# Kernel optimization log

Measured on AMD Instinct MI355X. Metric: run time of the kernel, lower is better.

Reference implementation:

```python
import jax, jax.numpy as jnp
import numpy as np

N = 100000   # nodes
E = 1600000  # edges (avg degree 16)
D = 128      # in_dim == hidden
L = 3        # num_layers
G = 512      # graphs in batch


def setup_inputs() -> dict:
    key = jax.random.key(0)
    ks = jax.random.split(key, 14)
    s = 0.05
    return {
        "x": jax.random.normal(ks[0], (N, D), jnp.float32),
        "edge_index": jax.random.randint(ks[1], (2, E), 0, N, dtype=jnp.int32),
        "batch": jnp.sort(jax.random.randint(ks[2], (N,), 0, G, dtype=jnp.int32)),
        "W1": jax.random.normal(ks[3], (L, D, D), jnp.float32) * s,
        "b1": jax.random.normal(ks[4], (L, D), jnp.float32) * s,
        "W2": jax.random.normal(ks[5], (L, D, D), jnp.float32) * s,
        "b2": jax.random.normal(ks[6], (L, D), jnp.float32) * s,
        "gamma": jax.random.uniform(ks[7], (L, D), jnp.float32, 0.5, 1.5),
        "beta": jax.random.normal(ks[8], (L, D), jnp.float32) * s,
        "run_mean": jax.random.normal(ks[9], (L, D), jnp.float32) * s,
        "run_var": jax.random.uniform(ks[10], (L, D), jnp.float32, 0.5, 1.5),
        "eps": jnp.zeros((L,), jnp.float32),
        "lin1_W": jax.random.normal(ks[11], (D, D), jnp.float32) * s,
        "lin1_b": jax.random.normal(ks[12], (D,), jnp.float32) * s,
    }


def _bn(h, g, b, m, v):
    # BatchNorm1d in eval mode (running stats)
    return (h - m) * jax.lax.rsqrt(v + 1e-5) * g + b


def reference(x, edge_index, batch, W1, b1, W2, b2, gamma, beta,
              run_mean, run_var, eps, lin1_W, lin1_b):
    n = x.shape[0]
    src, dst = edge_index[0], edge_index[1]
    h = x
    for l in range(L):  # small fixed layer count
        # GINConv: sum-aggregate neighbor features then (1+eps)*self + agg
        agg = jax.ops.segment_sum(h[src], dst, num_segments=n)  # [N, D]
        z = (1.0 + eps[l]) * h + agg
        z = jax.nn.relu(z @ W1[l] + b1[l])
        z = jax.nn.relu(z @ W2[l] + b2[l])
        h = _bn(z, gamma[l], beta[l], run_mean[l], run_var[l])
    # global_mean_pool over graph ids
    counts = jax.ops.segment_sum(jnp.ones((n,), h.dtype), batch, num_segments=G)
    pooled = jax.ops.segment_sum(h, batch, num_segments=G)
    pooled = pooled / jnp.maximum(counts, 1.0)[:, None]  # [G, D]
    # lin1 + ReLU (dropout is identity in eval)
    return jax.nn.relu(pooled @ lin1_W + lin1_b)
```

## Files before the change

kernel.cpp:

```cpp
#include <hip/hip_runtime.h>
#include <hip/hip_bf16.h>

#define NN 100000
#define NE 1600000
#define DD 128
#define NL 3
#define NG 512
#define NBLK ((NN + 255) / 256)
#define CSRP (NE + 8 * NN)

#define CONV_BLKS 12501
#define PREPW_BLKS 384
#define DEG_BLKS  391
#define INIT_BLKS (CONV_BLKS + PREPW_BLKS + DEG_BLKS)

typedef __attribute__((ext_vector_type(8))) short bf16x8;
typedef __attribute__((ext_vector_type(4))) float f32x4;

__device__ __forceinline__ unsigned short f2bf(float f) {
    union { float f; unsigned int u; } x; x.f = f;
    unsigned int r = x.u + 0x7FFFu + ((x.u >> 16) & 1u);
    return (unsigned short)(r >> 16);
}
__device__ __forceinline__ float bf2f(unsigned short u) {
    union { unsigned int u; float f; } x; x.u = ((unsigned int)u) << 16;
    return x.f;
}
__device__ __forceinline__ float bflo(unsigned int v) { return bf2f((unsigned short)(v & 0xffffu)); }
__device__ __forceinline__ float bfhi(unsigned int v) { return bf2f((unsigned short)(v >> 16)); }
__device__ __forceinline__ unsigned cvtpk(float lo, float hi) {
    unsigned r;
    asm("v_cvt_pk_bf16_f32 %0, %1, %2" : "=v"(r) : "v"(lo), "v"(hi));
    return r;
}

__global__ __launch_bounds__(256) void init_all(const float* __restrict__ x,
                                                unsigned short* __restrict__ h0,
                                                unsigned short* __restrict__ h1,
                                                const float* __restrict__ W1,
                                                const float* __restrict__ W2,
                                                unsigned short* __restrict__ wbf,
                                                int* __restrict__ deg) {
    int bb = blockIdx.x;
    if (bb < CONV_BLKS) {
        long long t = (long long)bb * 256 + threadIdx.x;
        long long base = t * 4;
        if (base < (long long)NN * DD) {
            float4 v = *reinterpret_cast<const float4*>(x + base);
            ushort4 p;
            p.x = f2bf(v.x); p.y = f2bf(v.y); p.z = f2bf(v.z); p.w = f2bf(v.w);
            *reinterpret_cast<ushort4*>(h0 + base) = p;
        } else if (base < (long long)(NN + 1) * DD) {
            ushort4 z = {0, 0, 0, 0};
            *reinterpret_cast<ushort4*>(h0 + base) = z;
            *reinterpret_cast<ushort4*>(h1 + base) = z;
        }
        return;
    }
    bb -= CONV_BLKS;
    if (bb < PREPW_BLKS) {
        int idx = bb * 256 + threadIdx.x;
        int k = idx & 127;
        int n = (idx >> 7) & 127;
        int w = (idx >> 14) & 1;
        int l = idx >> 15;
        const float* src = w ? W2 : W1;
        wbf[idx] = f2bf(src[(l * DD + k) * DD + n]);
        return;
    }
    bb -= PREPW_BLKS;
    int i = bb * 256 + threadIdx.x;
    if (i < NN) deg[i] = 0;
}

__global__ __launch_bounds__(256) void hist_deg(const int* __restrict__ ei,
                                                int* __restrict__ deg) {
    unsigned int e = blockIdx.x * 256u + threadIdx.x;
    atomicAdd(&deg[ei[NE + e]], 1);
}

__global__ __launch_bounds__(256) void scan1(const int* __restrict__ deg,
                                             int* __restrict__ rp,
                                             int* __restrict__ part) {
    __shared__ int s[256];
    int tid = threadIdx.x;
    int i = blockIdx.x * 256 + tid;
    int v = 0;
    if (i < NN) v = (deg[i] + 7) & ~7;
    s[tid] = v;
    __syncthreads();
    for (int o = 1; o < 256; o <<= 1) {
        int t = (tid >= o) ? s[tid - o] : 0;
        __syncthreads();
        s[tid] += t;
        __syncthreads();
    }
    if (i < NN) rp[i] = s[tid] - v;
    if (tid == 255) part[blockIdx.x] = s[255];
}

__global__ __launch_bounds__(256) void scan23(int* __restrict__ rp,
                                              const int* __restrict__ part,
                                              const int* __restrict__ deg,
                                              int* __restrict__ cnt,
                                              int* __restrict__ csr) {
    __shared__ int red[256];
    int tid = threadIdx.x;
    int bid = blockIdx.x;
    int s = 0;
    for (int i = tid; i < bid; i += 256) s += part[i];
    red[tid] = s;
    __syncthreads();
    for (int o = 128; o > 0; o >>= 1) {
        if (tid < o) red[tid] += red[tid + o];
        __syncthreads();
    }
    int base = red[0];
    int i = bid * 256 + tid;
    if (i < NN) {
        int val = rp[i] + base;
        rp[i] = val;
        cnt[i] = 0;
        int d = deg[i];
        int pd = (d + 7) & ~7;
        for (int j = val + d; j < val + pd; ++j) csr[j] = NN;
        if (i == NN - 1) rp[NN] = val + pd;
    }
}

__global__ __launch_bounds__(256) void fill_csr(const int* __restrict__ ei,
                                                const int* __restrict__ rp,
                                                int* __restrict__ cnt,
                                                int* __restrict__ csr) {
    unsigned int e = blockIdx.x * 256u + threadIdx.x;
    int s = ei[e];
    int d = ei[NE + e];
    int pos = atomicAdd(&cnt[d], 1);
    csr[rp[d] + pos] = s;
}

__global__ __launch_bounds__(256) void layer_fused(
    const unsigned short* __restrict__ hin,
    const int* __restrict__ rp,
    const int* __restrict__ csr,
    const unsigned short* __restrict__ w1t,
    const unsigned short* __restrict__ w2t,
    const float* __restrict__ b1,
    const float* __restrict__ b2,
    const float* __restrict__ gamma,
    const float* __restrict__ beta,
    const float* __restrict__ rmean,
    const float* __restrict__ rvar,
    const float* __restrict__ epsv,
    unsigned short* __restrict__ hout)
{
    __shared__ unsigned short z_lds[16 * 136];
    const int tid = threadIdx.x;
    const int lane = tid & 63;
    const int wave = tid >> 6;
    const int gid = lane >> 4;
    const int lg = lane & 15;
    const int row0 = blockIdx.x * 16;
    const float epl = 1.0f + epsv[0];
    const size_t lgo = (size_t)lg * 8;

#define ACC8(v) do { \
    acc[0] += bflo((v).x); acc[1] += bfhi((v).x); \
    acc[2] += bflo((v).y); acc[3] += bfhi((v).y); \
    acc[4] += bflo((v).z); acc[5] += bfhi((v).z); \
    acc[6] += bflo((v).w); acc[7] += bfhi((v).w); } while (0)

    const int rbase = row0 + (wave << 2);
    int pv = (lane < 5) ? rp[rbase + lane] : 0;
    const int st = __shfl(pv, gid);
    const int en = __shfl(pv, gid + 1);
    const int myrow = rbase + gid;

    float acc[8];
    {
        uint4 sv = *reinterpret_cast<const uint4*>(hin + (size_t)myrow * DD + lgo);
        acc[0] = epl * bflo(sv.x); acc[1] = epl * bfhi(sv.x);
        acc[2] = epl * bflo(sv.y); acc[3] = epl * bfhi(sv.y);
        acc[4] = epl * bflo(sv.z); acc[5] = epl * bfhi(sv.z);
        acc[6] = epl * bflo(sv.w); acc[7] = epl * bfhi(sv.w);
    }
    for (int c0 = st; c0 < en; c0 += 8) {
        int4 idA = *reinterpret_cast<const int4*>(csr + c0);
        int4 idB = *reinterpret_cast<const int4*>(csr + c0 + 4);
        uint4 v0 = *reinterpret_cast<const uint4*>(hin + (size_t)idA.x * DD + lgo);
        uint4 v1 = *reinterpret_cast<const uint4*>(hin + (size_t)idA.y * DD + lgo);
        uint4 v2 = *reinterpret_cast<const uint4*>(hin + (size_t)idA.z * DD + lgo);
        uint4 v3 = *reinterpret_cast<const uint4*>(hin + (size_t)idA.w * DD + lgo);
        uint4 v4 = *reinterpret_cast<const uint4*>(hin + (size_t)idB.x * DD + lgo);
        uint4 v5 = *reinterpret_cast<const uint4*>(hin + (size_t)idB.y * DD + lgo);
        uint4 v6 = *reinterpret_cast<const uint4*>(hin + (size_t)idB.z * DD + lgo);
        uint4 v7 = *reinterpret_cast<const uint4*>(hin + (size_t)idB.w * DD + lgo);
        ACC8(v0); ACC8(v1); ACC8(v2); ACC8(v3);
        ACC8(v4); ACC8(v5); ACC8(v6); ACC8(v7);
    }
    {
        uint4 pk;
        pk.x = cvtpk(acc[0], acc[1]);
        pk.y = cvtpk(acc[2], acc[3]);
        pk.z = cvtpk(acc[4], acc[5]);
        pk.w = cvtpk(acc[6], acc[7]);
        *reinterpret_cast<uint4*>(&z_lds[((wave << 2) + gid) * 136 + lg * 8]) = pk;
    }
    __syncthreads();

    const int l15 = lane & 15;
    const int kq = lane >> 4;
    const int colbase = wave << 5;

    bf16x8 afr[4];
    #pragma unroll
    for (int kk = 0; kk < 4; ++kk)
        afr[kk] = *reinterpret_cast<const bf16x8*>(&z_lds[l15 * 136 + kk * 32 + kq * 8]);

    f32x4 acc4[2];
    #pragma unroll
    for (int nt = 0; nt < 2; ++nt) acc4[nt] = (f32x4){0.f, 0.f, 0.f, 0.f};
    #pragma unroll
    for (int nt = 0; nt < 2; ++nt) {
        #pragma unroll
        for (int kk = 0; kk < 4; ++kk) {
            bf16x8 bfr = *reinterpret_cast<const bf16x8*>(
                w1t + (colbase + nt * 16 + l15) * DD + kk * 32 + kq * 8);
            acc4[nt] = __builtin_amdgcn_mfma_f32_16x16x32_bf16(afr[kk], bfr, acc4[nt], 0, 0, 0);
        }
    }
    __syncthreads();

    #pragma unroll
    for (int nt = 0; nt < 2; ++nt) {
        int col = colbase + nt * 16 + l15;
        float bv = b1[col];
        #pragma unroll
        for (int r = 0; r < 4; ++r) {
            int zr = kq * 4 + r;
            float v = acc4[nt][r] + bv;
            v = v > 0.f ? v : 0.f;
            z_lds[zr * 136 + col] = f2bf(v);
        }
    }
    __syncthreads();

    #pragma unroll
    for (int kk = 0; kk < 4; ++kk)
        afr[kk] = *reinterpret_cast<const bf16x8*>(&z_lds[l15 * 136 + kk * 32 + kq * 8]);
    #pragma unroll
    for (int nt = 0; nt < 2; ++nt) acc4[nt] = (f32x4){0.f, 0.f, 0.f, 0.f};
    #pragma unroll
    for (int nt = 0; nt < 2; ++nt) {
        #pragma unroll
        for (int kk = 0; kk < 4; ++kk) {
            bf16x8 bfr = *reinterpret_cast<const bf16x8*>(
                w2t + (colbase + nt * 16 + l15) * DD + kk * 32 + kq * 8);
            acc4[nt] = __builtin_amdgcn_mfma_f32_16x16x32_bf16(afr[kk], bfr, acc4[nt], 0, 0, 0);
        }
    }

    #pragma unroll
    for (int nt = 0; nt < 2; ++nt) {
        int col = colbase + nt * 16 + l15;
        float bv = b2[col];
        float ga = gamma[col];
        float be = beta[col];
        float mu = rmean[col];
        float inv = rsqrtf(rvar[col] + 1e-5f);
        #pragma unroll
        for (int r = 0; r < 4; ++r) {
            int zr = kq * 4 + r;
            float v = acc4[nt][r] + bv;
            v = v > 0.f ? v : 0.f;
            v = (v - mu) * inv * ga + be;
            hout[(size_t)(row0 + zr) * DD + col] = f2bf(v);
        }
    }
#undef ACC8
}

__global__ __launch_bounds__(256) void pool_final(const unsigned short* __restrict__ h,
                                                  const int* __restrict__ batch,
                                                  const float* __restrict__ W,
                                                  const float* __restrict__ b,
                                                  float* __restrict__ out) {
    int g = blockIdx.x;
    int t = threadIdx.x;
    int c2 = t & 63;
    int qu = t >> 6;

    int lo = 0, hi = NN;
    while (lo < hi) { int mid = (lo + hi) >> 1; if (batch[mid] < g) lo = mid + 1; else hi = mid; }
    int start = lo;
    hi = NN;
    while (lo < hi) { int mid = (lo + hi) >> 1; if (batch[mid] < g + 1) lo = mid + 1; else hi = mid; }
    int end = lo;

    float ax = 0.f, ay = 0.f;
    for (int i = start + qu; i < end; i += 4) {
        unsigned u = *reinterpret_cast<const unsigned*>(h + (size_t)i * DD + c2 * 2);
        ax += bflo(u); ay += bfhi(u);
    }

    __shared__ float ps[4][DD];
    ps[qu][c2 * 2] = ax;
    ps[qu][c2 * 2 + 1] = ay;
    __syncthreads();
    if (t < DD) {
        float inv = 1.0f / fmaxf((float)(end - start), 1.0f);
        ps[0][t] = (ps[0][t] + ps[1][t] + ps[2][t] + ps[3][t]) * inv;
    }
    __syncthreads();
    if (t < DD) {
        float o = b[t];
        #pragma unroll 8
        for (int k = 0; k < DD; ++k)
            o += ps[0][k] * W[k * DD + t];
        out[(size_t)g * DD + t] = fmaxf(o, 0.f);
    }
}

extern "C" void kernel_launch(void* const* d_in, const int* in_sizes, int n_in,
                              void* d_out, int out_size, void* d_ws, size_t ws_size,
                              hipStream_t stream) {
    const float* x     = (const float*)d_in[0];
    const int*   ei    = (const int*)d_in[1];
    const int*   batch = (const int*)d_in[2];
    const float* W1    = (const float*)d_in[3];
    const float* b1    = (const float*)d_in[4];
    const float* W2    = (const float*)d_in[5];
    const float* b2    = (const float*)d_in[6];
    const float* gamma = (const float*)d_in[7];
    const float* beta  = (const float*)d_in[8];
    const float* rmean = (const float*)d_in[9];
    const float* rvar  = (const float*)d_in[10];
    const float* eps   = (const float*)d_in[11];
    const float* lin1W = (const float*)d_in[12];
    const float* lin1b = (const float*)d_in[13];
    float* out = (float*)d_out;

    char* ws = (char*)d_ws;
    size_t off = 0;
    auto alloc = [&](size_t bytes) {
        void* p = ws + off;
        off = (off + bytes + 255) & ~(size_t)255;
        return p;
    };
    unsigned short* h0  = (unsigned short*)alloc((size_t)(NN + 1) * DD * 2);
    unsigned short* h1  = (unsigned short*)alloc((size_t)(NN + 1) * DD * 2);
    int* rp   = (int*)alloc((size_t)(NN + 1) * 4);
    int* deg  = (int*)alloc((size_t)NN * 4);
    int* cnt  = (int*)alloc((size_t)NN * 4);
    int* part = (int*)alloc(512 * 4);
    int* csr  = (int*)alloc((size_t)CSRP * 4);
    unsigned short* wbf = (unsigned short*)alloc((size_t)NL * 2 * DD * DD * 2);

    init_all<<<INIT_BLKS, 256, 0, stream>>>(x, h0, h1, W1, W2, wbf, deg);

    hist_deg<<<NE / 256, 256, 0, stream>>>(ei, deg);
    scan1<<<NBLK, 256, 0, stream>>>(deg, rp, part);
    scan23<<<NBLK, 256, 0, stream>>>(rp, part, deg, cnt, csr);
    fill_csr<<<NE / 256, 256, 0, stream>>>(ei, rp, cnt, csr);

    const int lgrid = NN / 16;
    layer_fused<<<lgrid, 256, 0, stream>>>(
        h0, rp, csr, wbf + 0 * DD * DD, wbf + 1 * DD * DD,
        b1 + 0 * DD, b2 + 0 * DD, gamma + 0 * DD, beta + 0 * DD,
        rmean + 0 * DD, rvar + 0 * DD, eps + 0, h1);
    layer_fused<<<lgrid, 256, 0, stream>>>(
        h1, rp, csr, wbf + 2 * DD * DD, wbf + 3 * DD * DD,
        b1 + 1 * DD, b2 + 1 * DD, gamma + 1 * DD, beta + 1 * DD,
        rmean + 1 * DD, rvar + 1 * DD, eps + 1, h0);
    layer_fused<<<lgrid, 256, 0, stream>>>(
        h0, rp, csr, wbf + 4 * DD * DD, wbf + 5 * DD * DD,
        b1 + 2 * DD, b2 + 2 * DD, gamma + 2 * DD, beta + 2 * DD,
        rmean + 2 * DD, rvar + 2 * DD, eps + 2, h1);

    pool_final<<<NG, 256, 0, stream>>>(h1, batch, lin1W, lin1b, out);
}
```

Baseline: 551.1 us.

## Build CSR via two-pass bucketed scatter with LDS atomics

Replaces the single fill_csr pass, which did a global atomic per edge on per-node counters followed by a random scatter, with a two-level scheme. Edges are first binned into buckets of 64 destination nodes using per-bucket global atomics into a staging buffer, then one block per bucket places edges into the CSR using shared-memory atomics. The aim is to cut global atomic contention and make the final CSR writes local to each bucket. In exchange it adds two kernel launches (one of them a single-block scan), an extra NE-sized buffer, and an extra read and write pass over all edges.

```diff
diff --git a/kernel.cpp b/kernel.cpp
--- a/kernel.cpp
+++ b/kernel.cpp
@@ -8,6 +8,7 @@
 #define NG 512
 #define NBLK ((NN + 255) / 256)
 #define CSRP (NE + 8 * NN)
+#define NBUCK ((NN + 63) / 64)
 
 #define CONV_BLKS 12501
 #define PREPW_BLKS 384
@@ -81,12 +82,13 @@
 
 __global__ __launch_bounds__(256) void scan1(const int* __restrict__ deg,
                                              int* __restrict__ rp,
-                                             int* __restrict__ part) {
+                                             int* __restrict__ part,
+                                             int* __restrict__ bhist) {
     __shared__ int s[256];
     int tid = threadIdx.x;
     int i = blockIdx.x * 256 + tid;
-    int v = 0;
-    if (i < NN) v = (deg[i] + 7) & ~7;
+    int vr = (i < NN) ? deg[i] : 0;
+    int v = (vr + 7) & ~7;
     s[tid] = v;
     __syncthreads();
     for (int o = 1; o < 256; o <<= 1) {
@@ -97,12 +99,16 @@
     }
     if (i < NN) rp[i] = s[tid] - v;
     if (tid == 255) part[blockIdx.x] = s[255];
+    int bs = vr;
+    #pragma unroll
+    for (int o = 1; o < 64; o <<= 1) bs += __shfl_xor(bs, o);
+    int bucket = blockIdx.x * 4 + (tid >> 6);
+    if ((tid & 63) == 0 && bucket < NBUCK) bhist[bucket] = bs;
 }
 
 __global__ __launch_bounds__(256) void scan23(int* __restrict__ rp,
                                               const int* __restrict__ part,
                                               const int* __restrict__ deg,
-                                              int* __restrict__ cnt,
                                               int* __restrict__ csr) {
     __shared__ int red[256];
     int tid = threadIdx.x;
@@ -120,7 +126,6 @@
     if (i < NN) {
         int val = rp[i] + base;
         rp[i] = val;
-        cnt[i] = 0;
         int d = deg[i];
         int pd = (d + 7) & ~7;
         for (int j = val + d; j < val + pd; ++j) csr[j] = NN;
@@ -128,15 +133,73 @@
     }
 }
 
-__global__ __launch_bounds__(256) void fill_csr(const int* __restrict__ ei,
-                                                const int* __restrict__ rp,
-                                                int* __restrict__ cnt,
-                                                int* __restrict__ csr) {
+__global__ __launch_bounds__(256) void bscan(const int* __restrict__ bhist,
+                                             int* __restrict__ boff,
+                                             int* __restrict__ bpos) {
+    __shared__ int s[256];
+    const int PT = (NBUCK + 255) / 256;
+    int tid = threadIdx.x;
+    int loc[PT];
+    int sum = 0;
+    #pragma unroll
+    for (int j = 0; j < PT; ++j) {
+        int idx = tid * PT + j;
+        int v = (idx < NBUCK) ? bhist[idx] : 0;
+        loc[j] = sum;
+        sum += v;
+    }
+    s[tid] = sum;
+    __syncthreads();
+    for (int o = 1; o < 256; o <<= 1) {
+        int t = (tid >= o) ? s[tid - o] : 0;
+        __syncthreads();
+        s[tid] += t;
+        __syncthreads();
+    }
+    int base = s[tid] - sum;
+    #pragma unroll
+    for (int j = 0; j < PT; ++j) {
+        int idx = tid * PT + j;
+        if (idx < NBUCK) boff[idx] = base + loc[j];
+    }
+    if (tid == 0) boff[NBUCK] = NE;
+    for (int i = tid; i < NBUCK; i += 256) bpos[i] = 0;
+}
+
+__global__ __launch_bounds__(256) void bin_scatter(const int* __restrict__ ei,
+                                                   const int* __restrict__ boff,
+                                                   int* __restrict__ bpos,
+                                                   int* __restrict__ ebuf) {
     unsigned int e = blockIdx.x * 256u + threadIdx.x;
     int s = ei[e];
     int d = ei[NE + e];
-    int pos = atomicAdd(&cnt[d], 1);
-    csr[rp[d] + pos] = s;
+    int b = d >> 6;
+    int pos = atomicAdd(&bpos[b], 1);
+    ebuf[boff[b] + pos] = s | ((d & 63) << 17);
+}
+
+__global__ __launch_bounds__(256) void fill2(const int* __restrict__ ebuf,
+                                             const int* __restrict__ boff,
+                                             const int* __restrict__ rp,
+                                             int* __restrict__ csr) {
+    __shared__ int lcnt[64];
+    __shared__ int rpl[64];
+    int b = blockIdx.x;
+    int tid = threadIdx.x;
+    if (tid < 64) {
+        int node = b * 64 + tid;
+        rpl[tid] = (node < NN) ? rp[node] : 0;
+        lcnt[tid] = 0;
+    }
+    __syncthreads();
+    int st = boff[b], en = boff[b + 1];
+    for (int i = st + tid; i < en; i += 256) {
+        int v = ebuf[i];
+        int s = v & 0x1FFFF;
+        int dl = v >> 17;
+        int pos = atomicAdd(&lcnt[dl], 1);
+        csr[rpl[dl] + pos] = s;
+    }
 }
 
 __global__ __launch_bounds__(256) void layer_fused(
@@ -349,19 +412,24 @@
     };
     unsigned short* h0  = (unsigned short*)alloc((size_t)(NN + 1) * DD * 2);
     unsigned short* h1  = (unsigned short*)alloc((size_t)(NN + 1) * DD * 2);
-    int* rp   = (int*)alloc((size_t)(NN + 1) * 4);
-    int* deg  = (int*)alloc((size_t)NN * 4);
-    int* cnt  = (int*)alloc((size_t)NN * 4);
-    int* part = (int*)alloc(512 * 4);
-    int* csr  = (int*)alloc((size_t)CSRP * 4);
+    int* rp    = (int*)alloc((size_t)(NN + 1) * 4);
+    int* deg   = (int*)alloc((size_t)NN * 4);
+    int* part  = (int*)alloc(512 * 4);
+    int* bhist = (int*)alloc((size_t)NBUCK * 4);
+    int* boff  = (int*)alloc((size_t)(NBUCK + 1) * 4);
+    int* bpos  = (int*)alloc((size_t)NBUCK * 4);
+    int* csr   = (int*)alloc((size_t)CSRP * 4);
+    int* ebuf  = (int*)alloc((size_t)NE * 4);
     unsigned short* wbf = (unsigned short*)alloc((size_t)NL * 2 * DD * DD * 2);
 
     init_all<<<INIT_BLKS, 256, 0, stream>>>(x, h0, h1, W1, W2, wbf, deg);
 
     hist_deg<<<NE / 256, 256, 0, stream>>>(ei, deg);
-    scan1<<<NBLK, 256, 0, stream>>>(deg, rp, part);
-    scan23<<<NBLK, 256, 0, stream>>>(rp, part, deg, cnt, csr);
-    fill_csr<<<NE / 256, 256, 0, stream>>>(ei, rp, cnt, csr);
+    scan1<<<NBLK, 256, 0, stream>>>(deg, rp, part, bhist);
+    scan23<<<NBLK, 256, 0, stream>>>(rp, part, deg, csr);
+    bscan<<<1, 256, 0, stream>>>(bhist, boff, bpos);
+    bin_scatter<<<NE / 256, 256, 0, stream>>>(ei, boff, bpos, ebuf);
+    fill2<<<NBUCK, 256, 0, stream>>>(ebuf, boff, rp, csr);
 
     const int lgrid = NN / 16;
     layer_fused<<<lgrid, 256, 0, stream>>>(
```

New measurement: 724.8 us. 31.5% more time.
